# Performance work log

Hardware: AMD Instinct MI355X
Metric: run time of the kernel (lower is better)

## Reference

```python
import jax, jax.numpy as jnp
import numpy as np

NUM_HEADS = 16


def setup_inputs() -> dict:
    key = jax.random.key(0)
    ks = jax.random.split(key, 9)
    B, Nq, Nk = 2, 2048, 2048
    qd, kd, vd = 1024, 1024, 1024
    s = 0.02
    return {
        "query": jax.random.normal(ks[0], (B, Nq, qd), jnp.float32),
        "key": jax.random.normal(ks[1], (B, Nk, kd), jnp.float32),
        "value": jax.random.normal(ks[2], (B, Nk, vd), jnp.float32),
        "Wq": jax.random.normal(ks[3], (qd, qd), jnp.float32) * s,
        "bq": jnp.zeros((qd,), jnp.float32),
        "Wk": jax.random.normal(ks[4], (kd, qd), jnp.float32) * s,
        "bk": jnp.zeros((qd,), jnp.float32),
        "Wv": jax.random.normal(ks[5], (vd, vd), jnp.float32) * s,
        "bv": jnp.zeros((vd,), jnp.float32),
    }


def _split_heads(x, num_heads):
    B, N, D = x.shape
    return x.reshape(B, N, num_heads, D // num_heads).transpose(0, 2, 1, 3)  # [B,H,N,depth]


def reference(query, key, value, Wq, bq, Wk, bk, Wv, bv):
    H = NUM_HEADS
    q = _split_heads(query @ Wq + bq, H)   # [B,H,Nq,dq]
    k = _split_heads(key @ Wk + bk, H)     # [B,H,Nk,dq]
    v = _split_heads(value @ Wv + bv, H)   # [B,H,Nk,dv]
    q_depth = q.shape[-1]
    scores = jnp.einsum('bhqd,bhkd->bhqk', q, k) / jnp.sqrt(jnp.float32(q_depth))
    scores = scores - jnp.max(scores, axis=-1, keepdims=True)
    attn = jax.nn.softmax(scores, axis=-1)  # [B,H,Nq,Nk]
    context = jnp.einsum('bhqk,bhkd->bhqd', attn, v)
    B, _, Nq, dv = context.shape
    context = context.transpose(0, 2, 1, 3).reshape(B, Nq, H * dv)
    return (context, attn)
```

## Files before the change

kernel.cpp:

```cpp
#include <hip/hip_runtime.h>
#include <hip/hip_bf16.h>
#include <stdint.h>

typedef __attribute__((ext_vector_type(4))) float floatx4;
typedef __attribute__((ext_vector_type(8))) short shortx8;

#define NTOK 2048
#define DMODEL 1024
#define NHEAD 16
#define DHEAD 64
#define BATCH 2

static __device__ __forceinline__ unsigned short f2bf(float f) {
    union { float f; unsigned int u; } v; v.f = f;
    return (unsigned short)((v.u + 0x7FFFu + ((v.u >> 16) & 1u)) >> 16);
}

static __device__ __forceinline__ floatx4 mfma16(shortx8 a, shortx8 b, floatx4 c) {
    return __builtin_amdgcn_mfma_f32_16x16x32_bf16(a, b, c, 0, 0, 0);
}

static __device__ __forceinline__ void gl_lds16(const unsigned short* g, unsigned short* l) {
    __builtin_amdgcn_global_load_lds(
        (const __attribute__((address_space(1))) unsigned int*)g,
        (__attribute__((address_space(3))) unsigned int*)l, 16, 0, 0);
}

#define C1 0.18033688f

__global__ void cast_x_kernel(const float* __restrict__ q, const float* __restrict__ k,
                              const float* __restrict__ v,
                              unsigned short* __restrict__ oq, unsigned short* __restrict__ ok,
                              unsigned short* __restrict__ ov) {
    const float* src = blockIdx.y == 0 ? q : (blockIdx.y == 1 ? k : v);
    unsigned short* dst = blockIdx.y == 0 ? oq : (blockIdx.y == 1 ? ok : ov);
    int i = (blockIdx.x * 256 + threadIdx.x) * 8;
    floatx4 a = *(const floatx4*)(src + i);
    floatx4 b = *(const floatx4*)(src + i + 4);
    union { shortx8 s; unsigned short u[8]; } o;
    o.u[0] = f2bf(a[0]); o.u[1] = f2bf(a[1]); o.u[2] = f2bf(a[2]); o.u[3] = f2bf(a[3]);
    o.u[4] = f2bf(b[0]); o.u[5] = f2bf(b[1]); o.u[6] = f2bf(b[2]); o.u[7] = f2bf(b[3]);
    *(shortx8*)(dst + i) = o.s;
}

__global__ void transpose_w_kernel(const float* __restrict__ wq, const float* __restrict__ wk,
                                   const float* __restrict__ wv,
                                   unsigned short* __restrict__ tq, unsigned short* __restrict__ tk,
                                   unsigned short* __restrict__ tv) {
    __shared__ float tile[32][33];
    const float* W = blockIdx.z == 0 ? wq : (blockIdx.z == 1 ? wk : wv);
    unsigned short* T = blockIdx.z == 0 ? tq : (blockIdx.z == 1 ? tk : tv);
    int tx = threadIdx.x, ty = threadIdx.y;
    int bx = blockIdx.x, by = blockIdx.y;
#pragma unroll
    for (int j = 0; j < 4; j++)
        tile[ty + j * 8][tx] = W[(by * 32 + ty + j * 8) * DMODEL + bx * 32 + tx];
    __syncthreads();
#pragma unroll
    for (int j = 0; j < 4; j++)
        T[(bx * 32 + ty + j * 8) * DMODEL + by * 32 + tx] = f2bf(tile[tx][ty + j * 8]);
}

__launch_bounds__(256)
__global__ void proj_gemm_kernel(const unsigned short* __restrict__ xq, const unsigned short* __restrict__ xk,
                                 const unsigned short* __restrict__ xv,
                                 const unsigned short* __restrict__ tq, const unsigned short* __restrict__ tk,
                                 const unsigned short* __restrict__ tv,
                                 const float* __restrict__ bq, const float* __restrict__ bk,
                                 const float* __restrict__ bv,
                                 unsigned short* __restrict__ qh, unsigned short* __restrict__ kh,
                                 unsigned short* __restrict__ vt) {
    int z = blockIdx.z;
    const unsigned short* X = z == 0 ? xq : (z == 1 ? xk : xv);
    const unsigned short* W = z == 0 ? tq : (z == 1 ? tk : tv);
    const float* bias = z == 0 ? bq : (z == 1 ? bk : bv);

    __shared__ unsigned short As[128 * 32];
    __shared__ unsigned short Bs[128 * 32];

    int t = threadIdx.x;
    int lane = t & 63, w = t >> 6;
    int wr = w >> 1, wc = w & 1;
    int r = lane & 15, g = lane >> 4;
    int m0 = blockIdx.y * 128, n0 = blockIdx.x * 128;

    floatx4 acc[4][4];
#pragma unroll
    for (int i = 0; i < 4; i++)
#pragma unroll
        for (int j = 0; j < 4; j++) acc[i][j] = (floatx4){0.f, 0.f, 0.f, 0.f};

    for (int kt = 0; kt < DMODEL; kt += 32) {
#pragma unroll
        for (int i = 0; i < 2; i++) {
            int idx = t + 256 * i;
            int row = idx >> 2, c8 = (idx & 3) * 8;
            gl_lds16(X + (size_t)(m0 + row) * DMODEL + kt + c8, As + idx * 8);
            gl_lds16(W + (size_t)(n0 + row) * DMODEL + kt + c8, Bs + idx * 8);
        }
        __syncthreads();
        shortx8 a[4], b[4];
#pragma unroll
        for (int f = 0; f < 4; f++) {
            a[f] = *(const shortx8*)(As + (wr * 64 + f * 16 + r) * 32 + g * 8);
            b[f] = *(const shortx8*)(Bs + (wc * 64 + f * 16 + r) * 32 + g * 8);
        }
#pragma unroll
        for (int fm = 0; fm < 4; fm++)
#pragma unroll
            for (int fn = 0; fn < 4; fn++)
                acc[fm][fn] = mfma16(a[fm], b[fn], acc[fm][fn]);
        __syncthreads();
    }

    unsigned short* dstQK = (z == 0) ? qh : kh;
#pragma unroll
    for (int fm = 0; fm < 4; fm++) {
#pragma unroll
        for (int fn = 0; fn < 4; fn++) {
            int n = n0 + wc * 64 + fn * 16 + r;
            float bval = bias[n];
            int h = n >> 6, d = n & 63;
#pragma unroll
            for (int reg = 0; reg < 4; reg++) {
                int m = m0 + wr * 64 + fm * 16 + g * 4 + reg;
                int bb = m >> 11, tok = m & 2047;
                unsigned short o = f2bf(acc[fm][fn][reg] + bval);
                if (z < 2)
                    dstQK[(((size_t)(bb * NHEAD + h) * NTOK + tok) * DHEAD) + d] = o;
                else
                    vt[(((size_t)(bb * NHEAD + h) * DHEAD + d) * NTOK) + tok] = o;
            }
        }
    }
}

__launch_bounds__(256, 4)
__global__ void attn_fused_kernel(const unsigned short* __restrict__ Qh,
                                  const unsigned short* __restrict__ Kh,
                                  const unsigned short* __restrict__ Vt,
                                  float* __restrict__ ctx, float* __restrict__ attn) {
    __shared__ __align__(16) unsigned short Kst[2][4096];
    __shared__ __align__(16) unsigned short Aux[2][4096];

    int t = threadIdx.x, lane = t & 63, w = t >> 6, r = lane & 15, g = lane >> 4;

    int bid = blockIdx.y * 64 + blockIdx.x;
    int xcd = bid & 7;
    int j = bid >> 3;
    int bh = xcd * 4 + (j & 3);
    int rest = j >> 2;
    int qb = rest >> 1;
    int role = rest & 1;

    int q0 = qb * 64 + w * 16;
    int qrow = q0 + r;
    int rs = r & 7;

    const unsigned short* Qp = Qh + ((size_t)bh * NTOK + q0) * DHEAD;
    const unsigned short* Kbase = Kh + (size_t)bh * NTOK * DHEAD;
    const unsigned short* Vbase = Vt + (size_t)bh * DHEAD * NTOK;

    shortx8 qf0 = *(const shortx8*)(Qp + r * DHEAD + g * 8);
    shortx8 qf1 = *(const shortx8*)(Qp + r * DHEAD + 32 + g * 8);

    const floatx4 zero = (floatx4){0.f, 0.f, 0.f, 0.f};

    auto STK = [&](int b, int it) {
#pragma unroll
        for (int p = 0; p < 2; ++p) {
            int row = p * 32 + (t >> 3);
            int cb = (t & 7) ^ ((t >> 3) & 7);
            gl_lds16(Kbase + ((size_t)(it * 64 + row)) * DHEAD + cb * 8,
                     Kst[b] + p * 2048 + t * 8);
        }
    };
    auto STV = [&](int b, int it) {
#pragma unroll
        for (int p = 0; p < 2; ++p) {
            int row = p * 32 + (t >> 3);
            int cb = (t & 7) ^ ((t >> 3) & 7);
            gl_lds16(Vbase + (size_t)row * NTOK + it * 64 + cb * 8,
                     Aux[b] + p * 2048 + t * 8);
        }
    };
    auto KF = [&](int b, int tq, int h) -> shortx8 {
        return *(const shortx8*)(Kst[b] + (tq * 16 + r) * 64 + 8 * (((h * 4) + g) ^ rs));
    };
    auto VF = [&](int b, int dt, int h4) -> shortx8 {
        return *(const shortx8*)(Aux[b] + (dt * 16 + r) * 64 + 8 * ((h4 + g) ^ rs));
    };

    if (role == 0) {
        floatx4 pv0 = zero, pv1 = zero, pv2 = zero, pv3 = zero;
        float sm = 0.f;
        const bool hi = (g >= 2);
        const int srcA = (r + ((g & 1) << 5)) << 2;
        const int srcB = srcA + 64;

        STK(0, 0); STV(0, 0);
        __syncthreads();
        for (int it = 0; it < 32; ++it) {
            int cur = it & 1, nxt = cur ^ 1;
            if (it < 31) { STK(nxt, it + 1); STV(nxt, it + 1); }
#pragma unroll
            for (int half = 0; half < 2; ++half) {
                unsigned int p01t0, p23t0, p01t1, p23t1;
                {
                    floatx4 sc = mfma16(KF(cur, half * 2, 0), qf0, zero);
                    sc = mfma16(KF(cur, half * 2, 1), qf1, sc);
                    float e0 = exp2f(C1 * sc[0]), e1 = exp2f(C1 * sc[1]);
                    float e2 = exp2f(C1 * sc[2]), e3 = exp2f(C1 * sc[3]);
                    sm += (e0 + e1) + (e2 + e3);
                    asm("v_cvt_pk_bf16_f32 %0, %1, %2" : "=v"(p01t0) : "v"(e0), "v"(e1));
                    asm("v_cvt_pk_bf16_f32 %0, %1, %2" : "=v"(p23t0) : "v"(e2), "v"(e3));
                }
                {
                    floatx4 sc = mfma16(KF(cur, half * 2 + 1, 0), qf0, zero);
                    sc = mfma16(KF(cur, half * 2 + 1, 1), qf1, sc);
                    float e0 = exp2f(C1 * sc[0]), e1 = exp2f(C1 * sc[1]);
                    float e2 = exp2f(C1 * sc[2]), e3 = exp2f(C1 * sc[3]);
                    sm += (e0 + e1) + (e2 + e3);
                    asm("v_cvt_pk_bf16_f32 %0, %1, %2" : "=v"(p01t1) : "v"(e0), "v"(e1));
                    asm("v_cvt_pk_bf16_f32 %0, %1, %2" : "=v"(p23t1) : "v"(e2), "v"(e3));
                }
                int b0a = __builtin_amdgcn_ds_bpermute(srcA, (int)p01t0);
                int b0b = __builtin_amdgcn_ds_bpermute(srcA, (int)p01t1);
                int b1a = __builtin_amdgcn_ds_bpermute(srcA, (int)p23t0);
                int b1b = __builtin_amdgcn_ds_bpermute(srcA, (int)p23t1);
                int b2a = __builtin_amdgcn_ds_bpermute(srcB, (int)p01t0);
                int b2b = __builtin_amdgcn_ds_bpermute(srcB, (int)p01t1);
                int b3a = __builtin_amdgcn_ds_bpermute(srcB, (int)p23t0);
                int b3b = __builtin_amdgcn_ds_bpermute(srcB, (int)p23t1);
                union { unsigned int u[4]; shortx8 s8; } pbu;
                pbu.u[0] = (unsigned)(hi ? b0b : b0a);
                pbu.u[1] = (unsigned)(hi ? b1b : b1a);
                pbu.u[2] = (unsigned)(hi ? b2b : b2a);
                pbu.u[3] = (unsigned)(hi ? b3b : b3a);
                pv0 = mfma16(VF(cur, 0, half * 4), pbu.s8, pv0);
                pv1 = mfma16(VF(cur, 1, half * 4), pbu.s8, pv1);
                pv2 = mfma16(VF(cur, 2, half * 4), pbu.s8, pv2);
                pv3 = mfma16(VF(cur, 3, half * 4), pbu.s8, pv3);
            }
            __syncthreads();
        }
        float tot = sm;
        tot += __shfl_xor(tot, 16, 64);
        tot += __shfl_xor(tot, 32, 64);
        float inv = 1.0f / tot;
        float* ctx_row =
            ctx + ((size_t)((bh >> 4) * NTOK + qrow)) * DMODEL + (bh & 15) * DHEAD + g * 4;
        *(floatx4*)(ctx_row) = pv0 * inv;
        *(floatx4*)(ctx_row + 16) = pv1 * inv;
        *(floatx4*)(ctx_row + 32) = pv2 * inv;
        *(floatx4*)(ctx_row + 48) = pv3 * inv;
    } else {
        float sm = 0.f;
        STK(0, 0);
        __syncthreads();
        for (int it = 0; it < 32; ++it) {
            int cur = it & 1, nxt = cur ^ 1;
            if (it < 31) STK(nxt, it + 1);
#pragma unroll
            for (int tq = 0; tq < 4; ++tq) {
                floatx4 sc = mfma16(KF(cur, tq, 0), qf0, zero);
                sc = mfma16(KF(cur, tq, 1), qf1, sc);
                sm += (exp2f(C1 * sc[0]) + exp2f(C1 * sc[1])) +
                      (exp2f(C1 * sc[2]) + exp2f(C1 * sc[3]));
            }
            __syncthreads();
        }
        float tot = sm;
        tot += __shfl_xor(tot, 16, 64);
        tot += __shfl_xor(tot, 32, 64);
        float nl2s = -__log2f(tot);

        float(*pw)[64] = (float(*)[64])((char*)Aux + (size_t)w * 4096);
        float* attn_base = attn + ((size_t)bh * NTOK + q0) * NTOK;

        STK(0, 0);
        __syncthreads();
        for (int it = 0; it < 32; ++it) {
            int cur = it & 1, nxt = cur ^ 1;
            if (it < 31) STK(nxt, it + 1);
            int kk0 = it * 64;
#pragma unroll
            for (int tq = 0; tq < 4; ++tq) {
                floatx4 sc = mfma16(KF(cur, tq, 0), qf0, zero);
                sc = mfma16(KF(cur, tq, 1), qf1, sc);
                float e0 = exp2f(fmaf(C1, sc[0], nl2s));
                float e1 = exp2f(fmaf(C1, sc[1], nl2s));
                float e2 = exp2f(fmaf(C1, sc[2], nl2s));
                float e3 = exp2f(fmaf(C1, sc[3], nl2s));
                int x_ = (tq * 4 + g) ^ r;
                *(floatx4*)&pw[r][4 * x_] = (floatx4){e0, e1, e2, e3};
            }
#pragma unroll
            for (int sID = 0; sID < 4; ++sID) {
                int row = 4 * sID + g;
                floatx4 vvv = *(const floatx4*)&pw[row][4 * (r ^ row)];
                __builtin_nontemporal_store(
                    vvv, (floatx4*)(attn_base + (size_t)row * NTOK + kk0 + 4 * r));
            }
            __syncthreads();
        }
    }
}

extern "C" void kernel_launch(void* const* d_in, const int* in_sizes, int n_in,
                              void* d_out, int out_size, void* d_ws, size_t ws_size,
                              hipStream_t stream) {
    const float* query = (const float*)d_in[0];
    const float* key   = (const float*)d_in[1];
    const float* value = (const float*)d_in[2];
    const float* Wq = (const float*)d_in[3];
    const float* bq = (const float*)d_in[4];
    const float* Wk = (const float*)d_in[5];
    const float* bk = (const float*)d_in[6];
    const float* Wv = (const float*)d_in[7];
    const float* bv = (const float*)d_in[8];

    const size_t NX = (size_t)BATCH * NTOK * DMODEL;
    const size_t NW = (size_t)DMODEL * DMODEL;

    unsigned short* ws = (unsigned short*)d_ws;
    unsigned short* Xq = ws;
    unsigned short* Xk = Xq + NX;
    unsigned short* Xv = Xk + NX;
    unsigned short* Tq = Xv + NX;
    unsigned short* Tk = Tq + NW;
    unsigned short* Tv = Tk + NW;
    unsigned short* Qh = Tv + NW;
    unsigned short* Kh = Qh + NX;
    unsigned short* Vt = Kh + NX;

    float* ctx = (float*)d_out;
    float* attn = ctx + NX;

    cast_x_kernel<<<dim3(2048, 3), 256, 0, stream>>>(query, key, value, Xq, Xk, Xv);
    transpose_w_kernel<<<dim3(32, 32, 3), dim3(32, 8), 0, stream>>>(Wq, Wk, Wv, Tq, Tk, Tv);
    proj_gemm_kernel<<<dim3(8, 32, 3), 256, 0, stream>>>(Xq, Xk, Xv, Tq, Tk, Tv,
                                                         bq, bk, bv, Qh, Kh, Vt);
    attn_fused_kernel<<<dim3(64, 32), 256, 0, stream>>>(Qh, Kh, Vt, ctx, attn);
}
```

Baseline: 251.6 us.

## Merge context and attention-write roles into one block per query tile

Previously each query tile was handled by two blocks: one computed P·V context along with the row sum, and the other recomputed the row sum in a separate pass before writing normalized attention. Now a single block computes the context and sum, then reuses that sum to write attention, which removes the redundant QK^T/exp sum pass and halves the grid to 1024 blocks. The cost is less parallelism: the context pass and the attention-write pass now run serially within one block instead of concurrently in separate blocks.

Measured after the change: 277.1 us. 1.1x slower.

```diff
diff --git a/kernel.cpp b/kernel.cpp
--- a/kernel.cpp
+++ b/kernel.cpp
@@ -136,22 +136,20 @@
 }
 
 __launch_bounds__(256, 4)
-__global__ void attn_fused_kernel(const unsigned short* __restrict__ Qh,
-                                  const unsigned short* __restrict__ Kh,
-                                  const unsigned short* __restrict__ Vt,
-                                  float* __restrict__ ctx, float* __restrict__ attn) {
+__global__ void attn2_kernel(const unsigned short* __restrict__ Qh,
+                             const unsigned short* __restrict__ Kh,
+                             const unsigned short* __restrict__ Vt,
+                             float* __restrict__ ctx, float* __restrict__ attn) {
     __shared__ __align__(16) unsigned short Kst[2][4096];
     __shared__ __align__(16) unsigned short Aux[2][4096];
 
     int t = threadIdx.x, lane = t & 63, w = t >> 6, r = lane & 15, g = lane >> 4;
 
-    int bid = blockIdx.y * 64 + blockIdx.x;
+    int bid = blockIdx.x;
     int xcd = bid & 7;
     int j = bid >> 3;
     int bh = xcd * 4 + (j & 3);
-    int rest = j >> 2;
-    int qb = rest >> 1;
-    int role = rest & 1;
+    int qb = j >> 2;
 
     int q0 = qb * 64 + w * 16;
     int qrow = q0 + r;
@@ -191,7 +189,8 @@
         return *(const shortx8*)(Aux[b] + (dt * 16 + r) * 64 + 8 * ((h4 + g) ^ rs));
     };
 
-    if (role == 0) {
+    float tot;
+    {
         floatx4 pv0 = zero, pv1 = zero, pv2 = zero, pv3 = zero;
         float sm = 0.f;
         const bool hi = (g >= 2);
@@ -244,7 +243,7 @@
             }
             __syncthreads();
         }
-        float tot = sm;
+        tot = sm;
         tot += __shfl_xor(tot, 16, 64);
         tot += __shfl_xor(tot, 32, 64);
         float inv = 1.0f / tot;
@@ -254,27 +253,11 @@
         *(floatx4*)(ctx_row + 16) = pv1 * inv;
         *(floatx4*)(ctx_row + 32) = pv2 * inv;
         *(floatx4*)(ctx_row + 48) = pv3 * inv;
-    } else {
-        float sm = 0.f;
-        STK(0, 0);
-        __syncthreads();
-        for (int it = 0; it < 32; ++it) {
-            int cur = it & 1, nxt = cur ^ 1;
-            if (it < 31) STK(nxt, it + 1);
-#pragma unroll
-            for (int tq = 0; tq < 4; ++tq) {
-                floatx4 sc = mfma16(KF(cur, tq, 0), qf0, zero);
-                sc = mfma16(KF(cur, tq, 1), qf1, sc);
-                sm += (exp2f(C1 * sc[0]) + exp2f(C1 * sc[1])) +
-                      (exp2f(C1 * sc[2]) + exp2f(C1 * sc[3]));
-            }
-            __syncthreads();
-        }
-        float tot = sm;
-        tot += __shfl_xor(tot, 16, 64);
-        tot += __shfl_xor(tot, 32, 64);
-        float nl2s = -__log2f(tot);
-
+    }
+
+    float nl2s = -__log2f(tot);
+
+    {
         float(*pw)[64] = (float(*)[64])((char*)Aux + (size_t)w * 4096);
         float* attn_base = attn + ((size_t)bh * NTOK + q0) * NTOK;
 
@@ -341,5 +324,5 @@
     transpose_w_kernel<<<dim3(32, 32, 3), dim3(32, 8), 0, stream>>>(Wq, Wk, Wv, Tq, Tk, Tv);
     proj_gemm_kernel<<<dim3(8, 32, 3), 256, 0, stream>>>(Xq, Xk, Xv, Tq, Tk, Tv,
                                                          bq, bk, bv, Qh, Kh, Vt);
-    attn_fused_kernel<<<dim3(64, 32), 256, 0, stream>>>(Qh, Kh, Vt, ctx, attn);
-}
+    attn2_kernel<<<dim3(1024), 256, 0, stream>>>(Qh, Kh, Vt, ctx, attn);
+}
```

## Write attention probabilities directly from registers and use partial vmcnt barriers

Applied to the files above, without the earlier changes.

Removes the LDS transpose staging of the softmax probabilities, so each lane stores its float4 of probabilities straight to global memory. It also replaces __syncthreads with a manual s_waitcnt vmcnt(4) plus s_barrier, so the loop waits only for the K-tile prefetch and not for the outstanding attn stores. This cuts LDS traffic and one barrier stall per iteration. In exchange the global stores are less coalesced: each row gets 16-byte chunks spread across lanes, and the nontemporal hint is dropped. The hand-tuned vmcnt count is fragile, because it depends on how many loads and stores the compiler issues per iteration.

Measured after the change: 271.9 us. +8.1%, slower.

```diff
diff --git a/kernel.cpp b/kernel.cpp
--- a/kernel.cpp
+++ b/kernel.cpp
@@ -275,11 +275,14 @@
         tot += __shfl_xor(tot, 32, 64);
         float nl2s = -__log2f(tot);
 
-        float(*pw)[64] = (float(*)[64])((char*)Aux + (size_t)w * 4096);
-        float* attn_base = attn + ((size_t)bh * NTOK + q0) * NTOK;
+        float* attn_row = attn + ((size_t)bh * NTOK + qrow) * NTOK;
 
         STK(0, 0);
-        __syncthreads();
+        asm volatile("s_waitcnt vmcnt(0)" ::: "memory");
+        __builtin_amdgcn_sched_barrier(0);
+        __builtin_amdgcn_s_barrier();
+        __builtin_amdgcn_sched_barrier(0);
+
         for (int it = 0; it < 32; ++it) {
             int cur = it & 1, nxt = cur ^ 1;
             if (it < 31) STK(nxt, it + 1);
@@ -288,21 +291,19 @@
             for (int tq = 0; tq < 4; ++tq) {
                 floatx4 sc = mfma16(KF(cur, tq, 0), qf0, zero);
                 sc = mfma16(KF(cur, tq, 1), qf1, sc);
-                float e0 = exp2f(fmaf(C1, sc[0], nl2s));
-                float e1 = exp2f(fmaf(C1, sc[1], nl2s));
-                float e2 = exp2f(fmaf(C1, sc[2], nl2s));
-                float e3 = exp2f(fmaf(C1, sc[3], nl2s));
-                int x_ = (tq * 4 + g) ^ r;
-                *(floatx4*)&pw[r][4 * x_] = (floatx4){e0, e1, e2, e3};
-            }
-#pragma unroll
-            for (int sID = 0; sID < 4; ++sID) {
-                int row = 4 * sID + g;
-                floatx4 vvv = *(const floatx4*)&pw[row][4 * (r ^ row)];
-                __builtin_nontemporal_store(
-                    vvv, (floatx4*)(attn_base + (size_t)row * NTOK + kk0 + 4 * r));
-            }
-            __syncthreads();
+                floatx4 e;
+                e[0] = exp2f(fmaf(C1, sc[0], nl2s));
+                e[1] = exp2f(fmaf(C1, sc[1], nl2s));
+                e[2] = exp2f(fmaf(C1, sc[2], nl2s));
+                e[3] = exp2f(fmaf(C1, sc[3], nl2s));
+                *(floatx4*)(attn_row + kk0 + tq * 16 + g * 4) = e;
+            }
+            if (it < 31) {
+                asm volatile("s_waitcnt vmcnt(4)" ::: "memory");
+                __builtin_amdgcn_sched_barrier(0);
+                __builtin_amdgcn_s_barrier();
+                __builtin_amdgcn_sched_barrier(0);
+            }
         }
     }
 }
```

## Split softmax row-sum pass into separate kernel before fused attention

Applied to the files above, without the earlier changes.

Moves the first pass of the attention-writing role (QK^T plus exp-sum per row) out of the fused attention kernel into a new sums_kernel that writes per-row sums to workspace. The attention kernel then reads the precomputed sum instead of recomputing it. The aim is to balance the two roles in the fused kernel, since the attn-writing blocks previously did two full QK passes. It adds a kernel launch and an extra workspace buffer, and the sum pass now runs serially before the fused kernel instead of concurrently with it.

Measured after the change: 289.9 us. 1.15x slower.

```diff
diff --git a/kernel.cpp b/kernel.cpp
--- a/kernel.cpp
+++ b/kernel.cpp
@@ -136,9 +136,69 @@
 }
 
 __launch_bounds__(256, 4)
+__global__ void sums_kernel(const unsigned short* __restrict__ Qh,
+                            const unsigned short* __restrict__ Kh,
+                            float* __restrict__ sums_p) {
+    __shared__ __align__(16) unsigned short Kst[2][4096];
+
+    int t = threadIdx.x, lane = t & 63, w = t >> 6, r = lane & 15, g = lane >> 4;
+
+    int bid = blockIdx.x;
+    int xcd = bid & 7;
+    int j = bid >> 3;
+    int bh = xcd * 4 + (j & 3);
+    int qb = j >> 2;
+
+    int q0 = qb * 64 + w * 16;
+    int rs = r & 7;
+
+    const unsigned short* Qp = Qh + ((size_t)bh * NTOK + q0) * DHEAD;
+    const unsigned short* Kbase = Kh + (size_t)bh * NTOK * DHEAD;
+
+    shortx8 qf0 = *(const shortx8*)(Qp + r * DHEAD + g * 8);
+    shortx8 qf1 = *(const shortx8*)(Qp + r * DHEAD + 32 + g * 8);
+
+    const floatx4 zero = (floatx4){0.f, 0.f, 0.f, 0.f};
+
+    auto STK = [&](int b, int it) {
+#pragma unroll
+        for (int p = 0; p < 2; ++p) {
+            int row = p * 32 + (t >> 3);
+            int cb = (t & 7) ^ ((t >> 3) & 7);
+            gl_lds16(Kbase + ((size_t)(it * 64 + row)) * DHEAD + cb * 8,
+                     Kst[b] + p * 2048 + t * 8);
+        }
+    };
+    auto KF = [&](int b, int tq, int h) -> shortx8 {
+        return *(const shortx8*)(Kst[b] + (tq * 16 + r) * 64 + 8 * (((h * 4) + g) ^ rs));
+    };
+
+    float sm = 0.f;
+    STK(0, 0);
+    __syncthreads();
+    for (int it = 0; it < 32; ++it) {
+        int cur = it & 1, nxt = cur ^ 1;
+        if (it < 31) STK(nxt, it + 1);
+#pragma unroll
+        for (int tq = 0; tq < 4; ++tq) {
+            floatx4 sc = mfma16(KF(cur, tq, 0), qf0, zero);
+            sc = mfma16(KF(cur, tq, 1), qf1, sc);
+            sm += (exp2f(C1 * sc[0]) + exp2f(C1 * sc[1])) +
+                  (exp2f(C1 * sc[2]) + exp2f(C1 * sc[3]));
+        }
+        __syncthreads();
+    }
+    float tot = sm;
+    tot += __shfl_xor(tot, 16, 64);
+    tot += __shfl_xor(tot, 32, 64);
+    if (lane < 16) sums_p[(size_t)bh * NTOK + q0 + r] = tot;
+}
+
+__launch_bounds__(256, 4)
 __global__ void attn_fused_kernel(const unsigned short* __restrict__ Qh,
                                   const unsigned short* __restrict__ Kh,
                                   const unsigned short* __restrict__ Vt,
+                                  const float* __restrict__ sums_p,
                                   float* __restrict__ ctx, float* __restrict__ attn) {
     __shared__ __align__(16) unsigned short Kst[2][4096];
     __shared__ __align__(16) unsigned short Aux[2][4096];
@@ -255,25 +315,8 @@
         *(floatx4*)(ctx_row + 32) = pv2 * inv;
         *(floatx4*)(ctx_row + 48) = pv3 * inv;
     } else {
-        float sm = 0.f;
-        STK(0, 0);
-        __syncthreads();
-        for (int it = 0; it < 32; ++it) {
-            int cur = it & 1, nxt = cur ^ 1;
-            if (it < 31) STK(nxt, it + 1);
-#pragma unroll
-            for (int tq = 0; tq < 4; ++tq) {
-                floatx4 sc = mfma16(KF(cur, tq, 0), qf0, zero);
-                sc = mfma16(KF(cur, tq, 1), qf1, sc);
-                sm += (exp2f(C1 * sc[0]) + exp2f(C1 * sc[1])) +
-                      (exp2f(C1 * sc[2]) + exp2f(C1 * sc[3]));
-            }
-            __syncthreads();
-        }
-        float tot = sm;
-        tot += __shfl_xor(tot, 16, 64);
-        tot += __shfl_xor(tot, 32, 64);
-        float nl2s = -__log2f(tot);
+        float s = sums_p[(size_t)bh * NTOK + qrow];
+        float nl2s = -__log2f(s);
 
         float(*pw)[64] = (float(*)[64])((char*)Aux + (size_t)w * 4096);
         float* attn_base = attn + ((size_t)bh * NTOK + q0) * NTOK;
@@ -333,6 +376,7 @@
     unsigned short* Qh = Tv + NW;
     unsigned short* Kh = Qh + NX;
     unsigned short* Vt = Kh + NX;
+    float* sums_p = (float*)(Vt + NX);
 
     float* ctx = (float*)d_out;
     float* attn = ctx + NX;
@@ -341,5 +385,6 @@
     transpose_w_kernel<<<dim3(32, 32, 3), dim3(32, 8), 0, stream>>>(Wq, Wk, Wv, Tq, Tk, Tv);
     proj_gemm_kernel<<<dim3(8, 32, 3), 256, 0, stream>>>(Xq, Xk, Xv, Tq, Tk, Tv,
                                                          bq, bk, bv, Qh, Kh, Vt);
-    attn_fused_kernel<<<dim3(64, 32), 256, 0, stream>>>(Qh, Kh, Vt, ctx, attn);
-}
+    sums_kernel<<<dim3(1024), 256, 0, stream>>>(Qh, Kh, sums_p);
+    attn_fused_kernel<<<dim3(64, 32), 256, 0, stream>>>(Qh, Kh, Vt, sums_p, ctx, attn);
+}
```
